# Performance work log

Measured on AMD Instinct MI355X. Metric: run time of the kernel, lower is better.

## Reference

```python
import jax, jax.numpy as jnp
import numpy as np

WS = 8          # window_size
NH = 6          # num_heads
C = 192         # in_channels
HD = C // NH    # head_dim
N = WS * WS     # tokens per window


def _relative_position_index(ws):
    coords = np.stack(np.meshgrid(np.arange(ws), np.arange(ws), indexing='ij'), axis=-1).reshape(-1, 2)
    rel = coords[:, None, :] - coords[None, :, :] + (ws - 1)  # [N,N,2] in [0, 2ws-2]
    return (rel[..., 0] * (2 * ws - 1) + rel[..., 1]).astype(np.int32)  # [N,N]


def setup_inputs() -> dict:
    key = jax.random.key(0)
    ks = jax.random.split(key, 10)
    s = 0.02
    B, H, W = 8, 128, 128
    inp = {
        'x': jax.random.normal(ks[0], (B, C, H, W), dtype=jnp.float32),
        'qkv_w': jax.random.normal(ks[1], (3 * C, C), dtype=jnp.float32) * s,
        'qkv_b': jnp.zeros((3 * C,), dtype=jnp.float32),
        'proj_w': jax.random.normal(ks[2], (C, C), dtype=jnp.float32) * s,
        'proj_b': jnp.zeros((C,), dtype=jnp.float32),
        'mlp1_w': jax.random.normal(ks[3], (2 * C, C), dtype=jnp.float32) * s,
        'mlp1_b': jnp.zeros((2 * C,), dtype=jnp.float32),
        'mlp2_w': jax.random.normal(ks[4], (C, C), dtype=jnp.float32) * s,
        'mlp2_b': jnp.zeros((C,), dtype=jnp.float32),
        'bias_table': jax.random.normal(ks[5], ((2 * WS - 1) ** 2,), dtype=jnp.float32) * s,
        'rel_index': jnp.asarray(_relative_position_index(WS)),
    }
    return inp


def reference(x, qkv_w, qkv_b, proj_w, proj_b, mlp1_w, mlp1_b, mlp2_w, mlp2_b, bias_table, rel_index):
    B, _, H, W = x.shape
    nwh, nww = H // WS, W // WS
    # ---- window partition: [B,C,H,W] -> [B*nWin, N, C]
    xw = x.reshape(B, C, nwh, WS, nww, WS).transpose(0, 2, 4, 3, 5, 1).reshape(-1, N, C)
    # ---- qkv projection
    qkv = xw @ qkv_w.T + qkv_b  # [Bn, N, 3C]
    q, k, v = jnp.split(qkv, 3, axis=-1)
    split_heads = lambda t: t.reshape(-1, N, NH, HD).transpose(0, 2, 1, 3)  # [Bn,NH,N,HD]
    q, k, v = split_heads(q), split_heads(k), split_heads(v)
    # ---- learned relative-position bias (WindowScoreBias), broadcast over batch & heads
    bias = bias_table[rel_index]  # [N,N]
    scores = jnp.einsum('bhnd,bhmd->bhnm', q, k) * (1.0 / jnp.sqrt(jnp.float32(HD))) + bias
    attn = jax.nn.softmax(scores, axis=-1)
    out = jnp.einsum('bhnm,bhmd->bhnd', attn, v)  # [Bn,NH,N,HD]
    out = out.transpose(0, 2, 1, 3).reshape(-1, N, C)
    out = out @ proj_w.T + proj_b
    # ---- window merge back to BCHW
    out = out.reshape(B, nwh, nww, WS, WS, C).transpose(0, 5, 1, 3, 2, 4).reshape(B, C, H, W)
    x = x + out  # residual 1
    # ---- pointwise GLU MLP (1x1 convs as channel einsums)
    h = jnp.einsum('bchw,oc->bohw', x, mlp1_w) + mlp1_b[None, :, None, None]
    a, b = jnp.split(h, 2, axis=1)
    g = a * jax.nn.sigmoid(b)
    m = jnp.einsum('bchw,oc->bohw', g, mlp2_w) + mlp2_b[None, :, None, None]
    return x + m  # residual 2
```

## Files before the change

kernel.cpp:

```cpp
#include <hip/hip_runtime.h>


typedef short          s16x8 __attribute__((ext_vector_type(8)));
typedef unsigned short u16x4 __attribute__((ext_vector_type(4)));
typedef unsigned short u16x8 __attribute__((ext_vector_type(8)));
typedef float          f32x4 __attribute__((ext_vector_type(4)));

#define MFMA(A, B, C) __builtin_amdgcn_mfma_f32_16x16x32_bf16((A), (B), (C), 0, 0, 0)

__device__ __forceinline__ unsigned short f2b(float f) {
  unsigned x = __float_as_uint(f);
  x = (x + 0x7FFFu + ((x >> 16) & 1u)) >> 16;
  return (unsigned short)x;
}
__device__ __forceinline__ float b2f(unsigned short u) {
  return __uint_as_float(((unsigned)u) << 16);
}

__device__ __forceinline__ int swz32(int t, int c) {
  return t * 32 + ((((c >> 3) ^ (t >> 1)) & 3) << 3) + (c & 7);
}
__device__ __forceinline__ int swz64(int t, int c) {
  return t * 64 + ((((c >> 3) ^ t) & 7) << 3) + (c & 7);
}

#define XSTR   200
#define WSLOT  37376
#define QSCALE 0.17677669529663687f

#define WOFF_QKV   0
#define WOFF_PROJ  110592
#define WOFF_MLP1  147456
#define WOFF_MLP2  221184
#define WOFF_BIASX_BYTES 516096
#define WOFF_YWIN_BYTES  532480

__global__ void prep_kernel(const float* __restrict__ qkv_w,
                            const float* __restrict__ proj_w,
                            const float* __restrict__ mlp1_w,
                            const float* __restrict__ mlp2_w,
                            const float* __restrict__ bias_table,
                            const int*   __restrict__ rel_index,
                            unsigned short* __restrict__ qkv_wb,
                            unsigned short* __restrict__ proj_wb,
                            unsigned short* __restrict__ mlp1_wb,
                            unsigned short* __restrict__ mlp2_wb,
                            float* __restrict__ biasx) {
  int j = blockIdx.x * 256 + threadIdx.x;
  if (j < 110592) {
    float v = qkv_w[j];
    if (j < 36864) v *= QSCALE;
    qkv_wb[j] = f2b(v);
  } else if (j < 147456) {
    proj_wb[j - 110592] = f2b(proj_w[j - 110592]);
  } else if (j < 221184) {
    mlp1_wb[j - 147456] = f2b(mlp1_w[j - 147456]);
  } else if (j < 258048) {
    mlp2_wb[j - 221184] = f2b(mlp2_w[j - 221184]);
  } else {
    int e = j - 258048;
    int l = e >> 6, v = e & 63;
    int tm = v >> 4, tn = (v >> 2) & 3, r = v & 3;
    int q = tn * 16 + (l & 15);
    int k = tm * 16 + (l >> 4) * 4 + r;
    biasx[e] = bias_table[rel_index[q * 64 + k]];
  }
}

__global__ __launch_bounds__(768, 3) void attn_kernel(
    const float* __restrict__ x,
    const unsigned short* __restrict__ qkv_wb, const float* __restrict__ qkv_b,
    const unsigned short* __restrict__ proj_wb, const float* __restrict__ proj_b,
    const float* __restrict__ biasx,
    unsigned short* __restrict__ y_win) {
  __shared__ __align__(16) unsigned short sm[2 * WSLOT];

  const int tid  = threadIdx.x;
  const int lane = tid & 63;
  const int wv   = tid >> 6;
  const int wid  = (wv >= 6) ? 1 : 0;
  const int hd   = wv - wid * 6;
  const int l15  = lane & 15;
  const int lg   = lane >> 4;
  const int pair = ((blockIdx.x & 7) << 7) | (blockIdx.x >> 3);
  const int wins0 = pair * 2;

  const float* xwb[2];
#pragma unroll
  for (int wi = 0; wi < 2; ++wi) {
    const int w = wins0 + wi;
    xwb[wi] = x + (size_t)(w >> 8) * 192 * 16384
                + (size_t)(((w >> 4) & 15) * 8) * 128 + (w & 15) * 8;
  }

#pragma unroll
  for (int it = 0; it < 4; ++it) {
    int job = tid + 768 * it;
    int wi = job / 1536;
    int j = job - wi * 1536;
    int c = j >> 3, i = j & 7;
    const float* src = xwb[wi] + (size_t)c * 16384 + i * 128;
    f32x4 v0 = *(const f32x4*)(src);
    f32x4 v1 = *(const f32x4*)(src + 4);
    unsigned short* dst = &sm[wi * WSLOT + (i * 8) * XSTR + c];
    dst[0 * XSTR] = f2b(v0[0]); dst[1 * XSTR] = f2b(v0[1]);
    dst[2 * XSTR] = f2b(v0[2]); dst[3 * XSTR] = f2b(v0[3]);
    dst[4 * XSTR] = f2b(v1[0]); dst[5 * XSTR] = f2b(v1[1]);
    dst[6 * XSTR] = f2b(v1[2]); dst[7 * XSTR] = f2b(v1[3]);
  }
  __syncthreads();

  unsigned short* xa = sm + wid * WSLOT;
  unsigned short* hb = xa + 12800 + hd * 4096;
  unsigned short* R0 = hb;
  unsigned short* R1 = hb + 2048;

  f32x4 accv[4][2];
#pragma unroll
  for (int nt = 0; nt < 2; ++nt) {
    const float bv = qkv_b[384 + hd * 32 + nt * 16 + l15];
#pragma unroll
    for (int m = 0; m < 4; ++m) accv[m][nt] = (f32x4){bv, bv, bv, bv};
  }
#pragma unroll
  for (int nt = 0; nt < 2; ++nt) {
    const int o = hd * 32 + nt * 16 + l15;
    const float bq = qkv_b[o] * QSCALE;
    const float bk = qkv_b[192 + o];
    f32x4 accq[4], acck[4];
#pragma unroll
    for (int m = 0; m < 4; ++m) {
      accq[m] = (f32x4){bq, bq, bq, bq};
      acck[m] = (f32x4){bk, bk, bk, bk};
    }
#pragma unroll
    for (int ks = 0; ks < 6; ++ks) {
      const int k0 = ks * 32 + lg * 8;
      s16x8 af[4];
#pragma unroll
      for (int m = 0; m < 4; ++m)
        af[m] = *(const s16x8*)&xa[(m * 16 + l15) * XSTR + k0];
      s16x8 wq  = *(const s16x8*)&qkv_wb[(size_t)o * 192 + k0];
      s16x8 wk  = *(const s16x8*)&qkv_wb[(size_t)(192 + o) * 192 + k0];
      s16x8 wvv = *(const s16x8*)&qkv_wb[(size_t)(384 + o) * 192 + k0];
#pragma unroll
      for (int m = 0; m < 4; ++m) {
        accq[m] = MFMA(af[m], wq, accq[m]);
        acck[m] = MFMA(af[m], wk, acck[m]);
        accv[m][nt] = MFMA(af[m], wvv, accv[m][nt]);
      }
    }
#pragma unroll
    for (int m = 0; m < 4; ++m)
#pragma unroll
      for (int r = 0; r < 4; ++r) {
        const int t = m * 16 + lg * 4 + r;
        const int d = nt * 16 + l15;
        R0[swz32(t, d)] = f2b(accq[m][r]);
        R1[swz32(t, d)] = f2b(acck[m][r]);
      }
  }
  u16x4 vreg[4][2];
#pragma unroll
  for (int m = 0; m < 4; ++m)
#pragma unroll
    for (int nt = 0; nt < 2; ++nt) {
      vreg[m][nt][0] = f2b(accv[m][nt][0]); vreg[m][nt][1] = f2b(accv[m][nt][1]);
      vreg[m][nt][2] = f2b(accv[m][nt][2]); vreg[m][nt][3] = f2b(accv[m][nt][3]);
    }

  const float* bxp = biasx + lane * 64;
  s16x8 kf[4], qf[4];
#pragma unroll
  for (int tm = 0; tm < 4; ++tm)
    kf[tm] = *(const s16x8*)&R1[swz32(tm * 16 + l15, lg * 8)];
#pragma unroll
  for (int tn = 0; tn < 4; ++tn)
    qf[tn] = *(const s16x8*)&R0[swz32(tn * 16 + l15, lg * 8)];
#pragma unroll
  for (int m = 0; m < 4; ++m)
#pragma unroll
    for (int nt = 0; nt < 2; ++nt)
      *(u16x4*)&R1[swz64(nt * 16 + l15, m * 16 + lg * 4)] = vreg[m][nt];

  f32x4 sc[4][4];
#pragma unroll
  for (int tm = 0; tm < 4; ++tm)
#pragma unroll
    for (int tn = 0; tn < 4; ++tn) {
      f32x4 bfr = *(const f32x4*)&bxp[tm * 16 + tn * 4];
      sc[tm][tn] = MFMA(kf[tm], qf[tn], bfr);
    }
#pragma unroll
  for (int tn = 0; tn < 4; ++tn) {
    float mx = sc[0][tn][0];
#pragma unroll
    for (int tm = 0; tm < 4; ++tm)
#pragma unroll
      for (int r = 0; r < 4; ++r) mx = fmaxf(mx, sc[tm][tn][r]);
    mx = fmaxf(mx, __shfl_xor(mx, 16));
    mx = fmaxf(mx, __shfl_xor(mx, 32));
    float sum = 0.f;
#pragma unroll
    for (int tm = 0; tm < 4; ++tm)
#pragma unroll
      for (int r = 0; r < 4; ++r) {
        float e = __expf(sc[tm][tn][r] - mx);
        sc[tm][tn][r] = e;
        sum += e;
      }
    sum += __shfl_xor(sum, 16);
    sum += __shfl_xor(sum, 32);
    const float inv = 1.0f / sum;
#pragma unroll
    for (int tm = 0; tm < 4; ++tm)
#pragma unroll
      for (int r = 0; r < 4; ++r) sc[tm][tn][r] *= inv;
  }

  f32x4 oacc[4][2];
#pragma unroll
  for (int m = 0; m < 4; ++m)
#pragma unroll
    for (int nt = 0; nt < 2; ++nt) oacc[m][nt] = (f32x4){0.f, 0.f, 0.f, 0.f};
#pragma unroll
  for (int half = 0; half < 2; ++half) {
#pragma unroll
    for (int tm = 0; tm < 2; ++tm)
#pragma unroll
      for (int tn = 0; tn < 4; ++tn) {
        u16x4 pv;
        pv[0] = f2b(sc[half * 2 + tm][tn][0]); pv[1] = f2b(sc[half * 2 + tm][tn][1]);
        pv[2] = f2b(sc[half * 2 + tm][tn][2]); pv[3] = f2b(sc[half * 2 + tm][tn][3]);
        *(u16x4*)&R0[swz32(tn * 16 + l15, tm * 16 + lg * 4)] = pv;
      }
    s16x8 ap[4], bv2[2];
#pragma unroll
    for (int m = 0; m < 4; ++m)
      ap[m] = *(const s16x8*)&R0[swz32(m * 16 + l15, lg * 8)];
#pragma unroll
    for (int nt = 0; nt < 2; ++nt)
      bv2[nt] = *(const s16x8*)&R1[swz64(nt * 16 + l15, half * 32 + lg * 8)];
#pragma unroll
    for (int m = 0; m < 4; ++m)
#pragma unroll
      for (int nt = 0; nt < 2; ++nt)
        oacc[m][nt] = MFMA(ap[m], bv2[nt], oacc[m][nt]);
  }
#pragma unroll
  for (int m = 0; m < 4; ++m)
#pragma unroll
    for (int nt = 0; nt < 2; ++nt) {
      const int d = nt * 16 + l15;
#pragma unroll
      for (int r = 0; r < 4; ++r)
        R0[swz32(m * 16 + lg * 4 + r, d)] = f2b(oacc[m][nt][r]);
    }
  __syncthreads();

  f32x4 pj[4][2];
#pragma unroll
  for (int nt = 0; nt < 2; ++nt) {
    const float bp = proj_b[hd * 32 + nt * 16 + l15];
#pragma unroll
    for (int m = 0; m < 4; ++m) pj[m][nt] = (f32x4){bp, bp, bp, bp};
  }
#pragma unroll
  for (int hh = 0; hh < 6; ++hh) {
    const unsigned short* aoh = xa + 12800 + hh * 4096;
    s16x8 aa[4];
#pragma unroll
    for (int m = 0; m < 4; ++m)
      aa[m] = *(const s16x8*)&aoh[swz32(m * 16 + l15, lg * 8)];
#pragma unroll
    for (int nt = 0; nt < 2; ++nt) {
      s16x8 wp = *(const s16x8*)&proj_wb[(size_t)(hd * 32 + nt * 16 + l15) * 192 + hh * 32 + lg * 8];
#pragma unroll
      for (int m = 0; m < 4; ++m) pj[m][nt] = MFMA(aa[m], wp, pj[m][nt]);
    }
  }
#pragma unroll
  for (int m = 0; m < 4; ++m)
#pragma unroll
    for (int nt = 0; nt < 2; ++nt) {
      const int o = hd * 32 + nt * 16 + l15;
#pragma unroll
      for (int r = 0; r < 4; ++r) {
        const int t = m * 16 + lg * 4 + r;
        xa[t * XSTR + o] = f2b(pj[m][nt][r] + b2f(xa[t * XSTR + o]));
      }
    }
  __syncthreads();
#pragma unroll
  for (int it = 0; it < 4; ++it) {
    int job = tid + 768 * it;
    int wi = job / 1536;
    int j = job - wi * 1536;
    int t = j / 24;
    int seg = j - t * 24;
    unsigned short* ywp = y_win + (size_t)(wins0 + wi) * 12288;
    *(u16x8*)&ywp[(size_t)j * 8] = *(const u16x8*)&sm[wi * WSLOT + t * XSTR + seg * 8];
  }
}

__global__ __launch_bounds__(256, 4) void mlp_kernel(
    const unsigned short* __restrict__ y_win,
    const unsigned short* __restrict__ w1b, const float* __restrict__ b1,
    const unsigned short* __restrict__ w2b, const float* __restrict__ b2,
    float* __restrict__ out) {
  __shared__ __align__(16) unsigned short sm2[2 * 64 * XSTR];
  unsigned short* yb = sm2;
  unsigned short* wk = sm2 + 64 * XSTR;

  const int tid  = threadIdx.x;
  const int lane = tid & 63;
  const int wv   = tid >> 6;
  const int l15  = lane & 15;
  const int lg   = lane >> 4;
  const int win  = ((blockIdx.x & 7) << 8) | (blockIdx.x >> 3);
  const int bb   = win >> 8;
  const int wh   = (win >> 4) & 15;
  const int wwi  = win & 15;

  const unsigned short* ywp = y_win + (size_t)win * 12288;
#pragma unroll
  for (int it = 0; it < 6; ++it) {
    int job = tid + 256 * it;
    int t = job / 24;
    int seg = job - t * 24;
    *(u16x8*)&yb[t * XSTR + seg * 8] = *(const u16x8*)&ywp[(size_t)job * 8];
  }
  __syncthreads();

#pragma unroll
  for (int i = 0; i < 3; ++i) {
    const int na = (3 * wv + i) * 16 + l15;
    const int nb = na + 192;
    f32x4 aacc[4], bacc[4];
    const float ba = b1[na], bbv = b1[nb];
#pragma unroll
    for (int m = 0; m < 4; ++m) {
      aacc[m] = (f32x4){ba, ba, ba, ba};
      bacc[m] = (f32x4){bbv, bbv, bbv, bbv};
    }
#pragma unroll
    for (int ks = 0; ks < 6; ++ks) {
      const int k0 = ks * 32 + lg * 8;
      s16x8 af[4];
#pragma unroll
      for (int m = 0; m < 4; ++m)
        af[m] = *(const s16x8*)&yb[(m * 16 + l15) * XSTR + k0];
      s16x8 wa = *(const s16x8*)&w1b[(size_t)na * 192 + k0];
      s16x8 wb = *(const s16x8*)&w1b[(size_t)nb * 192 + k0];
#pragma unroll
      for (int m = 0; m < 4; ++m) {
        aacc[m] = MFMA(af[m], wa, aacc[m]);
        bacc[m] = MFMA(af[m], wb, bacc[m]);
      }
    }
#pragma unroll
    for (int m = 0; m < 4; ++m)
#pragma unroll
      for (int r = 0; r < 4; ++r) {
        const float g = aacc[m][r] * (1.0f / (1.0f + __expf(-bacc[m][r])));
        wk[(m * 16 + lg * 4 + r) * XSTR + na] = f2b(g);
      }
  }
  __syncthreads();

  int ocol[3];
  f32x4 macc[4][3];
#pragma unroll
  for (int i = 0; i < 3; ++i) {
    ocol[i] = (3 * wv + i) * 16 + l15;
    const float bb2 = b2[ocol[i]];
#pragma unroll
    for (int m = 0; m < 4; ++m) macc[m][i] = (f32x4){bb2, bb2, bb2, bb2};
  }
#pragma unroll
  for (int ks = 0; ks < 6; ++ks) {
    const int k0 = ks * 32 + lg * 8;
    s16x8 gf[4];
#pragma unroll
    for (int m = 0; m < 4; ++m)
      gf[m] = *(const s16x8*)&wk[(m * 16 + l15) * XSTR + k0];
#pragma unroll
    for (int i = 0; i < 3; ++i) {
      s16x8 wf = *(const s16x8*)&w2b[(size_t)ocol[i] * 192 + k0];
#pragma unroll
      for (int m = 0; m < 4; ++m) macc[m][i] = MFMA(gf[m], wf, macc[m][i]);
    }
  }
  __syncthreads();
#pragma unroll
  for (int m = 0; m < 4; ++m)
#pragma unroll
    for (int i = 0; i < 3; ++i)
#pragma unroll
      for (int r = 0; r < 4; ++r)
        wk[(m * 16 + lg * 4 + r) * XSTR + ocol[i]] = f2b(macc[m][i][r]);
  __syncthreads();

  float* obase = out + (size_t)bb * 192 * 16384 + (size_t)(wh * 8) * 128 + wwi * 8;
#pragma unroll
  for (int it = 0; it < 6; ++it) {
    int job = tid + 256 * it;
    int i = job / 192;
    int c = job - i * 192;
    float vals[8];
#pragma unroll
    for (int j = 0; j < 8; ++j) {
      const int t = i * 8 + j;
      vals[j] = b2f(yb[t * XSTR + c]) + b2f(wk[t * XSTR + c]);
    }
    float* dst = obase + (size_t)c * 16384 + i * 128;
    f32x4 o0 = {vals[0], vals[1], vals[2], vals[3]};
    f32x4 o1 = {vals[4], vals[5], vals[6], vals[7]};
    *(f32x4*)dst = o0;
    *(f32x4*)(dst + 4) = o1;
  }
}

extern "C" void kernel_launch(void* const* d_in, const int* in_sizes, int n_in,
                              void* d_out, int out_size, void* d_ws, size_t ws_size,
                              hipStream_t stream) {
  (void)in_sizes; (void)n_in; (void)out_size; (void)ws_size;
  const float* x          = (const float*)d_in[0];
  const float* qkv_w      = (const float*)d_in[1];
  const float* qkv_b      = (const float*)d_in[2];
  const float* proj_w     = (const float*)d_in[3];
  const float* proj_b     = (const float*)d_in[4];
  const float* mlp1_w     = (const float*)d_in[5];
  const float* mlp1_b     = (const float*)d_in[6];
  const float* mlp2_w     = (const float*)d_in[7];
  const float* mlp2_b     = (const float*)d_in[8];
  const float* bias_table = (const float*)d_in[9];
  const int*   rel_index  = (const int*)d_in[10];
  float* out = (float*)d_out;

  char* ws = (char*)d_ws;
  unsigned short* qkv_wb  = (unsigned short*)ws + WOFF_QKV;
  unsigned short* proj_wb = (unsigned short*)ws + WOFF_PROJ;
  unsigned short* mlp1_wb = (unsigned short*)ws + WOFF_MLP1;
  unsigned short* mlp2_wb = (unsigned short*)ws + WOFF_MLP2;
  float*          biasx   = (float*)(ws + WOFF_BIASX_BYTES);
  unsigned short* y_win   = (unsigned short*)(ws + WOFF_YWIN_BYTES);

  hipLaunchKernelGGL(prep_kernel, dim3(1024), dim3(256), 0, stream,
                     qkv_w, proj_w, mlp1_w, mlp2_w, bias_table, rel_index,
                     qkv_wb, proj_wb, mlp1_wb, mlp2_wb, biasx);
  hipLaunchKernelGGL(attn_kernel, dim3(1024), dim3(768), 0, stream,
                     x, qkv_wb, qkv_b, proj_wb, proj_b, biasx, y_win);
  hipLaunchKernelGGL(mlp_kernel, dim3(2048), dim3(256), 0, stream,
                     y_win, mlp1_wb, mlp1_b, mlp2_wb, mlp2_b, out);
}
```

Baseline: 243.3 us.

## Transpose attention MFMAs and swizzle window smem to vectorize LDS stores

Swaps the MFMA operand order for the Q/K projection, the attention-times-V product and the output projection. Each lane now holds four consecutive head-dim or channel values and can write them as one 8-byte LDS store instead of four scalar scattered stores. It also XOR-swizzles the bf16 window tile in shared memory and changes the V layout swizzle to cut bank conflicts, and loads biases as vectors. All readers and writers of the window buffer are updated to use the new swizzle. The swizzle math has to stay consistent across every use, and the remapped XOR on column blocks must remain within the stride-200 row.

```diff
diff --git a/kernel.cpp b/kernel.cpp
--- a/kernel.cpp
+++ b/kernel.cpp
@@ -20,11 +20,15 @@
 __device__ __forceinline__ int swz32(int t, int c) {
   return t * 32 + ((((c >> 3) ^ (t >> 1)) & 3) << 3) + (c & 7);
 }
-__device__ __forceinline__ int swz64(int t, int c) {
-  return t * 64 + ((((c >> 3) ^ t) & 7) << 3) + (c & 7);
+__device__ __forceinline__ int swzV(int d, int t) {
+  return d * 64 + ((((t >> 3) ^ (d + (d >> 3))) & 7) << 3) + (t & 7);
 }
 
 #define XSTR   200
+__device__ __forceinline__ int xsw(int t, int c) {
+  return t * XSTR + ((((c >> 3) ^ ((t >> 3) & 7))) << 3) + (c & 7);
+}
+
 #define WSLOT  37376
 #define QSCALE 0.17677669529663687f
 
@@ -102,11 +106,11 @@
     const float* src = xwb[wi] + (size_t)c * 16384 + i * 128;
     f32x4 v0 = *(const f32x4*)(src);
     f32x4 v1 = *(const f32x4*)(src + 4);
-    unsigned short* dst = &sm[wi * WSLOT + (i * 8) * XSTR + c];
-    dst[0 * XSTR] = f2b(v0[0]); dst[1 * XSTR] = f2b(v0[1]);
-    dst[2 * XSTR] = f2b(v0[2]); dst[3 * XSTR] = f2b(v0[3]);
-    dst[4 * XSTR] = f2b(v1[0]); dst[5 * XSTR] = f2b(v1[1]);
-    dst[6 * XSTR] = f2b(v1[2]); dst[7 * XSTR] = f2b(v1[3]);
+    unsigned short* dst = &sm[wi * WSLOT + (((c >> 3) ^ i) << 3) + (c & 7)];
+    dst[(i * 8 + 0) * XSTR] = f2b(v0[0]); dst[(i * 8 + 1) * XSTR] = f2b(v0[1]);
+    dst[(i * 8 + 2) * XSTR] = f2b(v0[2]); dst[(i * 8 + 3) * XSTR] = f2b(v0[3]);
+    dst[(i * 8 + 4) * XSTR] = f2b(v1[0]); dst[(i * 8 + 5) * XSTR] = f2b(v1[1]);
+    dst[(i * 8 + 6) * XSTR] = f2b(v1[2]); dst[(i * 8 + 7) * XSTR] = f2b(v1[3]);
   }
   __syncthreads();
 
@@ -114,59 +118,73 @@
   unsigned short* hb = xa + 12800 + hd * 4096;
   unsigned short* R0 = hb;
   unsigned short* R1 = hb + 2048;
-
-  f32x4 accv[4][2];
+  const int oQ = hd * 32;
+
+  f32x4 accqT[2][4], acckT[2][4], accv[4][2];
+#pragma unroll
+  for (int m = 0; m < 2; ++m) {
+    f32x4 bq4 = *(const f32x4*)&qkv_b[oQ + m * 16 + lg * 4];
+    f32x4 bk4 = *(const f32x4*)&qkv_b[192 + oQ + m * 16 + lg * 4];
+#pragma unroll
+    for (int tn = 0; tn < 4; ++tn) {
+      accqT[m][tn] = bq4 * QSCALE;
+      acckT[m][tn] = bk4;
+    }
+  }
 #pragma unroll
   for (int nt = 0; nt < 2; ++nt) {
-    const float bv = qkv_b[384 + hd * 32 + nt * 16 + l15];
-#pragma unroll
-    for (int m = 0; m < 4; ++m) accv[m][nt] = (f32x4){bv, bv, bv, bv};
-  }
-#pragma unroll
-  for (int nt = 0; nt < 2; ++nt) {
-    const int o = hd * 32 + nt * 16 + l15;
-    const float bq = qkv_b[o] * QSCALE;
-    const float bk = qkv_b[192 + o];
-    f32x4 accq[4], acck[4];
-#pragma unroll
-    for (int m = 0; m < 4; ++m) {
-      accq[m] = (f32x4){bq, bq, bq, bq};
-      acck[m] = (f32x4){bk, bk, bk, bk};
-    }
-#pragma unroll
-    for (int ks = 0; ks < 6; ++ks) {
-      const int k0 = ks * 32 + lg * 8;
-      s16x8 af[4];
-#pragma unroll
-      for (int m = 0; m < 4; ++m)
-        af[m] = *(const s16x8*)&xa[(m * 16 + l15) * XSTR + k0];
-      s16x8 wq  = *(const s16x8*)&qkv_wb[(size_t)o * 192 + k0];
-      s16x8 wk  = *(const s16x8*)&qkv_wb[(size_t)(192 + o) * 192 + k0];
-      s16x8 wvv = *(const s16x8*)&qkv_wb[(size_t)(384 + o) * 192 + k0];
-#pragma unroll
-      for (int m = 0; m < 4; ++m) {
-        accq[m] = MFMA(af[m], wq, accq[m]);
-        acck[m] = MFMA(af[m], wk, acck[m]);
-        accv[m][nt] = MFMA(af[m], wvv, accv[m][nt]);
-      }
-    }
-#pragma unroll
-    for (int m = 0; m < 4; ++m)
+    const float bv = qkv_b[384 + oQ + nt * 16 + l15];
+#pragma unroll
+    for (int mt = 0; mt < 4; ++mt) accv[mt][nt] = (f32x4){bv, bv, bv, bv};
+  }
+#pragma unroll
+  for (int ks = 0; ks < 6; ++ks) {
+    const int k0 = ks * 32 + lg * 8;
+    s16x8 bf[4];
+#pragma unroll
+    for (int tn = 0; tn < 4; ++tn)
+      bf[tn] = *(const s16x8*)&xa[xsw(tn * 16 + l15, k0)];
+    s16x8 wq[2], wk[2], wvv[2];
+#pragma unroll
+    for (int m = 0; m < 2; ++m) {
+      wq[m] = *(const s16x8*)&qkv_wb[(size_t)(oQ + m * 16 + l15) * 192 + k0];
+      wk[m] = *(const s16x8*)&qkv_wb[(size_t)(192 + oQ + m * 16 + l15) * 192 + k0];
+      wvv[m] = *(const s16x8*)&qkv_wb[(size_t)(384 + oQ + m * 16 + l15) * 192 + k0];
+    }
+#pragma unroll
+    for (int m = 0; m < 2; ++m)
+#pragma unroll
+      for (int tn = 0; tn < 4; ++tn) {
+        accqT[m][tn] = MFMA(wq[m], bf[tn], accqT[m][tn]);
+        acckT[m][tn] = MFMA(wk[m], bf[tn], acckT[m][tn]);
+      }
+#pragma unroll
+    for (int mt = 0; mt < 4; ++mt)
+#pragma unroll
+      for (int nt = 0; nt < 2; ++nt)
+        accv[mt][nt] = MFMA(bf[mt], wvv[nt], accv[mt][nt]);
+  }
+#pragma unroll
+  for (int m = 0; m < 2; ++m)
+#pragma unroll
+    for (int tn = 0; tn < 4; ++tn) {
+      const int t = tn * 16 + l15, d0 = m * 16 + lg * 4;
+      u16x4 q4, k4;
 #pragma unroll
       for (int r = 0; r < 4; ++r) {
-        const int t = m * 16 + lg * 4 + r;
-        const int d = nt * 16 + l15;
-        R0[swz32(t, d)] = f2b(accq[m][r]);
-        R1[swz32(t, d)] = f2b(acck[m][r]);
-      }
-  }
+        q4[r] = f2b(accqT[m][tn][r]);
+        k4[r] = f2b(acckT[m][tn][r]);
+      }
+      *(u16x4*)&R0[swz32(t, d0)] = q4;
+      *(u16x4*)&R1[swz32(t, d0)] = k4;
+    }
   u16x4 vreg[4][2];
 #pragma unroll
-  for (int m = 0; m < 4; ++m)
+  for (int mt = 0; mt < 4; ++mt)
 #pragma unroll
     for (int nt = 0; nt < 2; ++nt) {
-      vreg[m][nt][0] = f2b(accv[m][nt][0]); vreg[m][nt][1] = f2b(accv[m][nt][1]);
-      vreg[m][nt][2] = f2b(accv[m][nt][2]); vreg[m][nt][3] = f2b(accv[m][nt][3]);
+      vreg[mt][nt][0] = f2b(accv[mt][nt][0]); vreg[mt][nt][1] = f2b(accv[mt][nt][1]);
+      vreg[mt][nt][2] = f2b(accv[mt][nt][2]); vreg[mt][nt][3] = f2b(accv[mt][nt][3]);
     }
 
   const float* bxp = biasx + lane * 64;
@@ -178,10 +196,10 @@
   for (int tn = 0; tn < 4; ++tn)
     qf[tn] = *(const s16x8*)&R0[swz32(tn * 16 + l15, lg * 8)];
 #pragma unroll
-  for (int m = 0; m < 4; ++m)
+  for (int mt = 0; mt < 4; ++mt)
 #pragma unroll
     for (int nt = 0; nt < 2; ++nt)
-      *(u16x4*)&R1[swz64(nt * 16 + l15, m * 16 + lg * 4)] = vreg[m][nt];
+      *(u16x4*)&R1[swzV(nt * 16 + l15, mt * 16 + lg * 4)] = vreg[mt][nt];
 
   f32x4 sc[4][4];
 #pragma unroll
@@ -218,77 +236,81 @@
       for (int r = 0; r < 4; ++r) sc[tm][tn][r] *= inv;
   }
 
-  f32x4 oacc[4][2];
-#pragma unroll
-  for (int m = 0; m < 4; ++m)
-#pragma unroll
-    for (int nt = 0; nt < 2; ++nt) oacc[m][nt] = (f32x4){0.f, 0.f, 0.f, 0.f};
+  f32x4 oT[2][4];
+#pragma unroll
+  for (int m = 0; m < 2; ++m)
+#pragma unroll
+    for (int tn = 0; tn < 4; ++tn) oT[m][tn] = (f32x4){0.f, 0.f, 0.f, 0.f};
 #pragma unroll
   for (int half = 0; half < 2; ++half) {
 #pragma unroll
     for (int tm = 0; tm < 2; ++tm)
 #pragma unroll
       for (int tn = 0; tn < 4; ++tn) {
-        u16x4 pv;
-        pv[0] = f2b(sc[half * 2 + tm][tn][0]); pv[1] = f2b(sc[half * 2 + tm][tn][1]);
-        pv[2] = f2b(sc[half * 2 + tm][tn][2]); pv[3] = f2b(sc[half * 2 + tm][tn][3]);
-        *(u16x4*)&R0[swz32(tn * 16 + l15, tm * 16 + lg * 4)] = pv;
-      }
-    s16x8 ap[4], bv2[2];
-#pragma unroll
-    for (int m = 0; m < 4; ++m)
-      ap[m] = *(const s16x8*)&R0[swz32(m * 16 + l15, lg * 8)];
-#pragma unroll
-    for (int nt = 0; nt < 2; ++nt)
-      bv2[nt] = *(const s16x8*)&R1[swz64(nt * 16 + l15, half * 32 + lg * 8)];
-#pragma unroll
-    for (int m = 0; m < 4; ++m)
-#pragma unroll
-      for (int nt = 0; nt < 2; ++nt)
-        oacc[m][nt] = MFMA(ap[m], bv2[nt], oacc[m][nt]);
-  }
-#pragma unroll
-  for (int m = 0; m < 4; ++m)
-#pragma unroll
-    for (int nt = 0; nt < 2; ++nt) {
-      const int d = nt * 16 + l15;
-#pragma unroll
-      for (int r = 0; r < 4; ++r)
-        R0[swz32(m * 16 + lg * 4 + r, d)] = f2b(oacc[m][nt][r]);
-    }
-  __syncthreads();
-
-  f32x4 pj[4][2];
-#pragma unroll
-  for (int nt = 0; nt < 2; ++nt) {
-    const float bp = proj_b[hd * 32 + nt * 16 + l15];
-#pragma unroll
-    for (int m = 0; m < 4; ++m) pj[m][nt] = (f32x4){bp, bp, bp, bp};
+        u16x4 p4;
+#pragma unroll
+        for (int r = 0; r < 4; ++r) p4[r] = f2b(sc[half * 2 + tm][tn][r]);
+        *(u16x4*)&R0[swz32(tn * 16 + l15, tm * 16 + lg * 4)] = p4;
+      }
+    s16x8 bp[4], av[2];
+#pragma unroll
+    for (int tn = 0; tn < 4; ++tn)
+      bp[tn] = *(const s16x8*)&R0[swz32(tn * 16 + l15, lg * 8)];
+#pragma unroll
+    for (int m = 0; m < 2; ++m)
+      av[m] = *(const s16x8*)&R1[swzV(m * 16 + l15, half * 32 + lg * 8)];
+#pragma unroll
+    for (int m = 0; m < 2; ++m)
+#pragma unroll
+      for (int tn = 0; tn < 4; ++tn)
+        oT[m][tn] = MFMA(av[m], bp[tn], oT[m][tn]);
+  }
+#pragma unroll
+  for (int m = 0; m < 2; ++m)
+#pragma unroll
+    for (int tn = 0; tn < 4; ++tn) {
+      u16x4 a4;
+#pragma unroll
+      for (int r = 0; r < 4; ++r) a4[r] = f2b(oT[m][tn][r]);
+      *(u16x4*)&R0[swz32(tn * 16 + l15, m * 16 + lg * 4)] = a4;
+    }
+  __syncthreads();
+
+  f32x4 pjT[2][4];
+#pragma unroll
+  for (int m = 0; m < 2; ++m) {
+    f32x4 bp4 = *(const f32x4*)&proj_b[oQ + m * 16 + lg * 4];
+#pragma unroll
+    for (int tn = 0; tn < 4; ++tn) pjT[m][tn] = bp4;
   }
 #pragma unroll
   for (int hh = 0; hh < 6; ++hh) {
     const unsigned short* aoh = xa + 12800 + hh * 4096;
     s16x8 aa[4];
 #pragma unroll
-    for (int m = 0; m < 4; ++m)
-      aa[m] = *(const s16x8*)&aoh[swz32(m * 16 + l15, lg * 8)];
-#pragma unroll
-    for (int nt = 0; nt < 2; ++nt) {
-      s16x8 wp = *(const s16x8*)&proj_wb[(size_t)(hd * 32 + nt * 16 + l15) * 192 + hh * 32 + lg * 8];
-#pragma unroll
-      for (int m = 0; m < 4; ++m) pj[m][nt] = MFMA(aa[m], wp, pj[m][nt]);
-    }
-  }
-#pragma unroll
-  for (int m = 0; m < 4; ++m)
-#pragma unroll
-    for (int nt = 0; nt < 2; ++nt) {
-      const int o = hd * 32 + nt * 16 + l15;
-#pragma unroll
-      for (int r = 0; r < 4; ++r) {
-        const int t = m * 16 + lg * 4 + r;
-        xa[t * XSTR + o] = f2b(pj[m][nt][r] + b2f(xa[t * XSTR + o]));
-      }
+    for (int tn = 0; tn < 4; ++tn)
+      aa[tn] = *(const s16x8*)&aoh[swz32(tn * 16 + l15, lg * 8)];
+    s16x8 wp[2];
+#pragma unroll
+    for (int m = 0; m < 2; ++m)
+      wp[m] = *(const s16x8*)&proj_wb[(size_t)(oQ + m * 16 + l15) * 192 + hh * 32 + lg * 8];
+#pragma unroll
+    for (int m = 0; m < 2; ++m)
+#pragma unroll
+      for (int tn = 0; tn < 4; ++tn)
+        pjT[m][tn] = MFMA(wp[m], aa[tn], pjT[m][tn]);
+  }
+#pragma unroll
+  for (int m = 0; m < 2; ++m)
+#pragma unroll
+    for (int tn = 0; tn < 4; ++tn) {
+      const int t = tn * 16 + l15, o0 = oQ + m * 16 + lg * 4;
+      const int ad = xsw(t, o0);
+      u16x4 old = *(const u16x4*)&xa[ad];
+      u16x4 nw;
+#pragma unroll
+      for (int r = 0; r < 4; ++r) nw[r] = f2b(pjT[m][tn][r] + b2f(old[r]));
+      *(u16x4*)&xa[ad] = nw;
     }
   __syncthreads();
 #pragma unroll
@@ -299,7 +321,7 @@
     int t = j / 24;
     int seg = j - t * 24;
     unsigned short* ywp = y_win + (size_t)(wins0 + wi) * 12288;
-    *(u16x8*)&ywp[(size_t)j * 8] = *(const u16x8*)&sm[wi * WSLOT + t * XSTR + seg * 8];
+    *(u16x8*)&ywp[(size_t)j * 8] = *(const u16x8*)&sm[wi * WSLOT + xsw(t, seg * 8)];
   }
 }
 
```

After: 236.1 us. 1.03x faster.
